# Optimization experiments

Hardware: AMD Instinct MI355X
Metric: run time of the kernel (lower is better)

Reference implementation:

```python
import jax, jax.numpy as jnp
import numpy as np

B, I, S = 1024, 128, 512
UNFOLDS = 6


def setup_inputs() -> dict:
    key = jax.random.key(0)
    ks = jax.random.split(key, 16)
    inputs = jax.random.normal(ks[0], (B, I), dtype=jnp.float32)
    hx = jax.random.normal(ks[1], (B, S), dtype=jnp.float32)
    # learned parameters, initialized per _get_variables()
    input_w = jnp.ones((I,), dtype=jnp.float32)
    input_b = jnp.zeros((I,), dtype=jnp.float32)
    sensory_mu = jax.random.uniform(ks[2], (I, S)) * 0.5 + 0.3
    sensory_sigma = jax.random.uniform(ks[3], (I, S)) * 5.0 + 3.0
    sensory_W = jax.random.uniform(ks[4], (I, S), minval=0.01, maxval=1.0)
    sensory_erev = (2.0 * jax.random.randint(ks[5], (I, S), 0, 2) - 1.0).astype(jnp.float32)
    mu = jax.random.uniform(ks[6], (S, S)) * 0.5 + 0.3
    sigma = jax.random.uniform(ks[7], (S, S)) * 5.0 + 3.0
    W = jax.random.uniform(ks[8], (S, S), minval=0.01, maxval=1.0)
    erev = (2.0 * jax.random.randint(ks[9], (S, S), 0, 2) - 1.0).astype(jnp.float32)
    vleak = jax.random.uniform(ks[10], (S,)) * 0.4 - 0.2
    gleak = jnp.ones((S,), dtype=jnp.float32)   # gleak_init_min == gleak_init_max == 1
    cm_t = jnp.full((S,), 0.5, dtype=jnp.float32)  # cm_init_min == cm_init_max == 0.5
    return dict(inputs=inputs, hx=hx, input_w=input_w, input_b=input_b,
                sensory_mu=sensory_mu, sensory_sigma=sensory_sigma,
                sensory_W=sensory_W, sensory_erev=sensory_erev,
                mu=mu, sigma=sigma, W=W, erev=erev,
                vleak=vleak, gleak=gleak, cm_t=cm_t)


def reference(inputs, hx, input_w, input_b, sensory_mu, sensory_sigma,
              sensory_W, sensory_erev, mu, sigma, W, erev, vleak, gleak, cm_t):
    # Affine input mapping
    x = inputs * input_w + input_b                      # [B, I]
    # Sensory synapse activation (computed once): [B, I, S]
    sens_act = sensory_W * jax.nn.sigmoid(sensory_sigma * (x[:, :, None] - sensory_mu))
    w_num_sensory = jnp.sum(sens_act * sensory_erev, axis=1)  # [B, S]
    w_den_sensory = jnp.sum(sens_act, axis=1)                 # [B, S]

    v = hx
    for _ in range(UNFOLDS):
        # Recurrent synapse activation: broadcast state over presynaptic dim -> [B, S, S]
        w_act = W * jax.nn.sigmoid(sigma * (v[:, :, None] - mu))
        w_num = jnp.sum(w_act * erev, axis=1) + w_num_sensory   # [B, S]
        w_den = jnp.sum(w_act, axis=1) + w_den_sensory          # [B, S]
        numerator = cm_t * v + gleak * vleak + w_num
        denominator = cm_t + gleak + w_den
        v = numerator / denominator
    # forward returns (outputs, next_state), which are the same tensor
    return v
```

## Files before the change

### kernel.cpp

```cpp
#include <hip/hip_runtime.h>
#include <hip/hip_bf16.h>


#define B_TOT 1024
#define I_DIM 128
#define S_DIM 512
#define UNFOLDS 6
#define BT 4

#if __has_builtin(__builtin_amdgcn_exp2f)
__device__ __forceinline__ float fast_exp2(float x) { return __builtin_amdgcn_exp2f(x); }
#else
__device__ __forceinline__ float fast_exp2(float x) {
    float r; asm("v_exp_f32 %0, %1" : "=v"(r) : "v"(x)); return r;
}
#endif

#if __has_builtin(__builtin_amdgcn_rcpf)
__device__ __forceinline__ float fast_rcp(float x) { return __builtin_amdgcn_rcpf(x); }
#else
__device__ __forceinline__ float fast_rcp(float x) {
    float r; asm("v_rcp_f32 %0, %1" : "=v"(r) : "v"(x)); return r;
}
#endif

__global__ __launch_bounds__(256) void prep_kernel(
    const float* __restrict__ sens_mu, const float* __restrict__ sens_sigma,
    const float* __restrict__ sens_W, const float* __restrict__ sens_erev,
    const float* __restrict__ mu, const float* __restrict__ sigma,
    const float* __restrict__ W, const float* __restrict__ erev,
    float4* __restrict__ recP, float4* __restrict__ sensP)
{
    const float L2E = 1.4426950408889634f;
    int idx = blockIdx.x * 256 + threadIdx.x;
    if (idx < I_DIM * S_DIM) {
        float sg = sens_sigma[idx], m = sens_mu[idx], w = sens_W[idx], er = sens_erev[idx];
        sensP[idx] = make_float4(-sg * L2E, sg * m * L2E, w * er, w);
    }
    if (idx < S_DIM * S_DIM) {
        float sg = sigma[idx], m = mu[idx], w = W[idx], er = erev[idx];
        recP[idx] = make_float4(-sg * L2E, sg * m * L2E, w * er, w);
    }
}

__global__ __launch_bounds__(512, 2) void liquid_main(
    const float* __restrict__ inputs,
    const float* __restrict__ hx,
    const float* __restrict__ input_w,
    const float* __restrict__ input_b,
    const float4* __restrict__ sensP,
    const float4* __restrict__ recP,
    const float* __restrict__ vleak,
    const float* __restrict__ gleak,
    const float* __restrict__ cm_t,
    float* __restrict__ out)
{
    const int j = threadIdx.x;
    const int b0 = blockIdx.x * BT;

    __shared__ float xs[BT][I_DIM];
    __shared__ float vs[BT][S_DIM];

    {
        int b = threadIdx.x >> 7, ii = threadIdx.x & 127;
        xs[b][ii] = inputs[(b0 + b) * I_DIM + ii] * input_w[ii] + input_b[ii];
    }
    #pragma unroll
    for (int k = 0; k < BT; ++k)
        vs[k][j] = hx[(b0 + k) * S_DIM + j];
    __syncthreads();

    float snum[BT], sden[BT];
    #pragma unroll
    for (int b = 0; b < BT; ++b) { snum[b] = 0.f; sden[b] = 0.f; }

    for (int i = 0; i < I_DIM; i += 4) {
        float4 p[4];
        #pragma unroll
        for (int u = 0; u < 4; ++u) p[u] = sensP[(i + u) * S_DIM + j];
        #pragma unroll
        for (int b = 0; b < BT; ++b) {
            float4 xv4 = *(const float4*)&xs[b][i];
            float xv[4] = {xv4.x, xv4.y, xv4.z, xv4.w};
            #pragma unroll
            for (int u = 0; u < 4; ++u) {
                float t = fmaf(p[u].x, xv[u], p[u].y);
                float e = fast_exp2(t);
                float s = fast_rcp(1.0f + e);
                snum[b] = fmaf(p[u].z, s, snum[b]);
                sden[b] = fmaf(p[u].w, s, sden[b]);
            }
        }
    }

    const float gl = gleak[j], vl = vleak[j], cmj = cm_t[j];
    const float glvl = gl * vl;
    const float cg = cmj + gl;

    for (int it = 0; it < UNFOLDS; ++it) {
        float num[BT], den[BT];
        #pragma unroll
        for (int b = 0; b < BT; ++b) { num[b] = snum[b]; den[b] = sden[b]; }

        for (int i = 0; i < S_DIM; i += 4) {
            float4 p[4];
            #pragma unroll
            for (int u = 0; u < 4; ++u) p[u] = recP[(i + u) * S_DIM + j];
            #pragma unroll
            for (int b = 0; b < BT; ++b) {
                float4 vv4 = *(const float4*)&vs[b][i];
                float vv[4] = {vv4.x, vv4.y, vv4.z, vv4.w};
                #pragma unroll
                for (int u = 0; u < 4; ++u) {
                    float t = fmaf(p[u].x, vv[u], p[u].y);
                    float e = fast_exp2(t);
                    float s = fast_rcp(1.0f + e);
                    num[b] = fmaf(p[u].z, s, num[b]);
                    den[b] = fmaf(p[u].w, s, den[b]);
                }
            }
        }

        float vnew[BT];
        #pragma unroll
        for (int b = 0; b < BT; ++b) {
            float vold = vs[b][j];
            vnew[b] = (fmaf(cmj, vold, glvl) + num[b]) / (cg + den[b]);
        }
        __syncthreads();
        #pragma unroll
        for (int b = 0; b < BT; ++b) vs[b][j] = vnew[b];
        __syncthreads();
    }

    #pragma unroll
    for (int b = 0; b < BT; ++b)
        out[(b0 + b) * S_DIM + j] = vs[b][j];
}

extern "C" void kernel_launch(void* const* d_in, const int* in_sizes, int n_in,
                              void* d_out, int out_size, void* d_ws, size_t ws_size,
                              hipStream_t stream) {
    const float* inputs   = (const float*)d_in[0];
    const float* hx       = (const float*)d_in[1];
    const float* input_w  = (const float*)d_in[2];
    const float* input_b  = (const float*)d_in[3];
    const float* s_mu     = (const float*)d_in[4];
    const float* s_sigma  = (const float*)d_in[5];
    const float* s_W      = (const float*)d_in[6];
    const float* s_erev   = (const float*)d_in[7];
    const float* mu       = (const float*)d_in[8];
    const float* sigma    = (const float*)d_in[9];
    const float* W        = (const float*)d_in[10];
    const float* erev     = (const float*)d_in[11];
    const float* vleak    = (const float*)d_in[12];
    const float* gleak    = (const float*)d_in[13];
    const float* cm_t     = (const float*)d_in[14];
    float* out = (float*)d_out;

    float4* recP  = (float4*)d_ws;
    float4* sensP = (float4*)((char*)d_ws + (size_t)S_DIM * S_DIM * sizeof(float4));

    int prep_threads = S_DIM * S_DIM;
    prep_kernel<<<(prep_threads + 255) / 256, 256, 0, stream>>>(
        s_mu, s_sigma, s_W, s_erev, mu, sigma, W, erev, recP, sensP);

    liquid_main<<<B_TOT / BT, S_DIM, 0, stream>>>(
        inputs, hx, input_w, input_b, sensP, recP, vleak, gleak, cm_t, out);
}
```

Before: 401.3 us.

## Pack synapse parameters as fp16 pairs and replace rcp with Newton iteration

The prep kernel packs two presynaptic rows of precomputed sigmoid parameters into half2 fields, halving the bytes streamed per synapse in the sensory and recurrent loops. The main loops prefetch the next parameter group into registers one step ahead. The hardware reciprocal is replaced with a bit-trick initial guess refined by two Newton steps, moving work off the transcendental unit onto FMAs. The trade-off is fp16 rounding of the parameters and extra conversion and ALU instructions.

```diff
diff --git a/kernel.cpp b/kernel.cpp
--- a/kernel.cpp
+++ b/kernel.cpp
@@ -1,5 +1,5 @@
 #include <hip/hip_runtime.h>
-#include <hip/hip_bf16.h>
+#include <hip/hip_fp16.h>
 
 
 #define B_TOT 1024
@@ -8,38 +8,76 @@
 #define UNFOLDS 6
 #define BT 4
 
+__device__ __forceinline__ float fexp2(float x) {
 #if __has_builtin(__builtin_amdgcn_exp2f)
-__device__ __forceinline__ float fast_exp2(float x) { return __builtin_amdgcn_exp2f(x); }
+    return __builtin_amdgcn_exp2f(x);
 #else
-__device__ __forceinline__ float fast_exp2(float x) {
     float r; asm("v_exp_f32 %0, %1" : "=v"(r) : "v"(x)); return r;
-}
 #endif
-
-#if __has_builtin(__builtin_amdgcn_rcpf)
-__device__ __forceinline__ float fast_rcp(float x) { return __builtin_amdgcn_rcpf(x); }
-#else
-__device__ __forceinline__ float fast_rcp(float x) {
-    float r; asm("v_rcp_f32 %0, %1" : "=v"(r) : "v"(x)); return r;
-}
-#endif
+}
+
+__device__ __forceinline__ float rcp_nr(float d) {
+    float y = __int_as_float(0x7EF311C3 - __float_as_int(d));
+    y = y * fmaf(-d, y, 2.0f);
+    y = y * fmaf(-d, y, 2.0f);
+    return y;
+}
+
+__device__ __forceinline__ __half2 u2h(unsigned int u) {
+    return __builtin_bit_cast(__half2, u);
+}
+
+__device__ __forceinline__ void sigpair(const uint4 p, float v0, float v1,
+                                        float& num, float& den) {
+    __half2 A  = u2h(p.x), C = u2h(p.y), Wn = u2h(p.z), Wp = u2h(p.w);
+    float t0 = fmaf(__low2float(A),  v0, __low2float(C));
+    float t1 = fmaf(__high2float(A), v1, __high2float(C));
+    float s0 = rcp_nr(1.0f + fexp2(t0));
+    float s1 = rcp_nr(1.0f + fexp2(t1));
+    num = fmaf(__low2float(Wn),  s0, num);
+    den = fmaf(__low2float(Wp),  s0, den);
+    num = fmaf(__high2float(Wn), s1, num);
+    den = fmaf(__high2float(Wp), s1, den);
+}
 
 __global__ __launch_bounds__(256) void prep_kernel(
     const float* __restrict__ sens_mu, const float* __restrict__ sens_sigma,
     const float* __restrict__ sens_W, const float* __restrict__ sens_erev,
     const float* __restrict__ mu, const float* __restrict__ sigma,
     const float* __restrict__ W, const float* __restrict__ erev,
-    float4* __restrict__ recP, float4* __restrict__ sensP)
+    uint4* __restrict__ recPP, uint4* __restrict__ sensPP)
 {
     const float L2E = 1.4426950408889634f;
     int idx = blockIdx.x * 256 + threadIdx.x;
-    if (idx < I_DIM * S_DIM) {
-        float sg = sens_sigma[idx], m = sens_mu[idx], w = sens_W[idx], er = sens_erev[idx];
-        sensP[idx] = make_float4(-sg * L2E, sg * m * L2E, w * er, w);
-    }
-    if (idx < S_DIM * S_DIM) {
-        float sg = sigma[idx], m = mu[idx], w = W[idx], er = erev[idx];
-        recP[idx] = make_float4(-sg * L2E, sg * m * L2E, w * er, w);
+    int j = idx & (S_DIM - 1);
+    int p = idx >> 9;
+    if (idx < (S_DIM / 2) * S_DIM) {
+        int i0 = 2 * p, i1 = 2 * p + 1;
+        float sg0 = sigma[i0 * S_DIM + j], sg1 = sigma[i1 * S_DIM + j];
+        float m0  = mu[i0 * S_DIM + j],    m1  = mu[i1 * S_DIM + j];
+        float w0  = W[i0 * S_DIM + j],     w1  = W[i1 * S_DIM + j];
+        float e0  = erev[i0 * S_DIM + j],  e1  = erev[i1 * S_DIM + j];
+        __half2 A  = __floats2half2_rn(-sg0 * L2E, -sg1 * L2E);
+        __half2 C  = __floats2half2_rn(sg0 * m0 * L2E, sg1 * m1 * L2E);
+        __half2 Wn = __floats2half2_rn(w0 * e0, w1 * e1);
+        __half2 Wp = __floats2half2_rn(w0, w1);
+        recPP[p * S_DIM + j] = make_uint4(
+            __builtin_bit_cast(unsigned int, A),  __builtin_bit_cast(unsigned int, C),
+            __builtin_bit_cast(unsigned int, Wn), __builtin_bit_cast(unsigned int, Wp));
+    }
+    if (idx < (I_DIM / 2) * S_DIM) {
+        int i0 = 2 * p, i1 = 2 * p + 1;
+        float sg0 = sens_sigma[i0 * S_DIM + j], sg1 = sens_sigma[i1 * S_DIM + j];
+        float m0  = sens_mu[i0 * S_DIM + j],    m1  = sens_mu[i1 * S_DIM + j];
+        float w0  = sens_W[i0 * S_DIM + j],     w1  = sens_W[i1 * S_DIM + j];
+        float e0  = sens_erev[i0 * S_DIM + j],  e1  = sens_erev[i1 * S_DIM + j];
+        __half2 A  = __floats2half2_rn(-sg0 * L2E, -sg1 * L2E);
+        __half2 C  = __floats2half2_rn(sg0 * m0 * L2E, sg1 * m1 * L2E);
+        __half2 Wn = __floats2half2_rn(w0 * e0, w1 * e1);
+        __half2 Wp = __floats2half2_rn(w0, w1);
+        sensPP[p * S_DIM + j] = make_uint4(
+            __builtin_bit_cast(unsigned int, A),  __builtin_bit_cast(unsigned int, C),
+            __builtin_bit_cast(unsigned int, Wn), __builtin_bit_cast(unsigned int, Wp));
     }
 }
 
@@ -48,8 +86,8 @@
     const float* __restrict__ hx,
     const float* __restrict__ input_w,
     const float* __restrict__ input_b,
-    const float4* __restrict__ sensP,
-    const float4* __restrict__ recP,
+    const uint4* __restrict__ sensPP,
+    const uint4* __restrict__ recPP,
     const float* __restrict__ vleak,
     const float* __restrict__ gleak,
     const float* __restrict__ cm_t,
@@ -74,22 +112,20 @@
     #pragma unroll
     for (int b = 0; b < BT; ++b) { snum[b] = 0.f; sden[b] = 0.f; }
 
-    for (int i = 0; i < I_DIM; i += 4) {
-        float4 p[4];
-        #pragma unroll
-        for (int u = 0; u < 4; ++u) p[u] = sensP[(i + u) * S_DIM + j];
-        #pragma unroll
-        for (int b = 0; b < BT; ++b) {
-            float4 xv4 = *(const float4*)&xs[b][i];
-            float xv[4] = {xv4.x, xv4.y, xv4.z, xv4.w};
+    {
+        const uint4* colS = sensPP + j;
+        uint4 a0 = colS[0 * S_DIM], a1 = colS[1 * S_DIM];
+        for (int g = 0; g < I_DIM / 4; ++g) {
+            int gn = (g + 1) & (I_DIM / 4 - 1);
+            uint4 n0 = colS[(2 * gn) * S_DIM];
+            uint4 n1 = colS[(2 * gn + 1) * S_DIM];
             #pragma unroll
-            for (int u = 0; u < 4; ++u) {
-                float t = fmaf(p[u].x, xv[u], p[u].y);
-                float e = fast_exp2(t);
-                float s = fast_rcp(1.0f + e);
-                snum[b] = fmaf(p[u].z, s, snum[b]);
-                sden[b] = fmaf(p[u].w, s, sden[b]);
+            for (int b = 0; b < BT; ++b) {
+                float4 xv = *(const float4*)&xs[b][4 * g];
+                sigpair(a0, xv.x, xv.y, snum[b], sden[b]);
+                sigpair(a1, xv.z, xv.w, snum[b], sden[b]);
             }
+            a0 = n0; a1 = n1;
         }
     }
 
@@ -97,28 +133,24 @@
     const float glvl = gl * vl;
     const float cg = cmj + gl;
 
+    const uint4* colR = recPP + j;
     for (int it = 0; it < UNFOLDS; ++it) {
         float num[BT], den[BT];
         #pragma unroll
         for (int b = 0; b < BT; ++b) { num[b] = snum[b]; den[b] = sden[b]; }
 
-        for (int i = 0; i < S_DIM; i += 4) {
-            float4 p[4];
-            #pragma unroll
-            for (int u = 0; u < 4; ++u) p[u] = recP[(i + u) * S_DIM + j];
+        uint4 a0 = colR[0 * S_DIM], a1 = colR[1 * S_DIM];
+        for (int g = 0; g < S_DIM / 4; ++g) {
+            int gn = (g + 1) & (S_DIM / 4 - 1);
+            uint4 n0 = colR[(2 * gn) * S_DIM];
+            uint4 n1 = colR[(2 * gn + 1) * S_DIM];
             #pragma unroll
             for (int b = 0; b < BT; ++b) {
-                float4 vv4 = *(const float4*)&vs[b][i];
-                float vv[4] = {vv4.x, vv4.y, vv4.z, vv4.w};
-                #pragma unroll
-                for (int u = 0; u < 4; ++u) {
-                    float t = fmaf(p[u].x, vv[u], p[u].y);
-                    float e = fast_exp2(t);
-                    float s = fast_rcp(1.0f + e);
-                    num[b] = fmaf(p[u].z, s, num[b]);
-                    den[b] = fmaf(p[u].w, s, den[b]);
-                }
+                float4 vv = *(const float4*)&vs[b][4 * g];
+                sigpair(a0, vv.x, vv.y, num[b], den[b]);
+                sigpair(a1, vv.z, vv.w, num[b], den[b]);
             }
+            a0 = n0; a1 = n1;
         }
 
         float vnew[BT];
@@ -158,13 +190,13 @@
     const float* cm_t     = (const float*)d_in[14];
     float* out = (float*)d_out;
 
-    float4* recP  = (float4*)d_ws;
-    float4* sensP = (float4*)((char*)d_ws + (size_t)S_DIM * S_DIM * sizeof(float4));
-
-    int prep_threads = S_DIM * S_DIM;
+    uint4* recPP  = (uint4*)d_ws;
+    uint4* sensPP = (uint4*)((char*)d_ws + (size_t)(S_DIM / 2) * S_DIM * sizeof(uint4));
+
+    int prep_threads = (S_DIM / 2) * S_DIM;
     prep_kernel<<<(prep_threads + 255) / 256, 256, 0, stream>>>(
-        s_mu, s_sigma, s_W, s_erev, mu, sigma, W, erev, recP, sensP);
+        s_mu, s_sigma, s_W, s_erev, mu, sigma, W, erev, recPP, sensPP);
 
     liquid_main<<<B_TOT / BT, S_DIM, 0, stream>>>(
-        inputs, hx, input_w, input_b, sensP, recP, vleak, gleak, cm_t, out);
-}
+        inputs, hx, input_w, input_b, sensPP, recPP, vleak, gleak, cm_t, out);
+}
```

New measurement: 448.9 us. 1.12x slower.
